# Kernel tuning notes

Measured on AMD Instinct MI355X. Metric: run time of the kernel, lower is better.

The kernel has to match this reference:

```python
import jax, jax.numpy as jnp
import numpy as np

RES = 32  # voxel resolution (init_kwargs)


def setup_inputs() -> dict:
    key = jax.random.key(0)
    k1, k2 = jax.random.split(key)
    B, C, N = 8, 64, 100000
    features = jax.random.normal(k1, (B, C, N), dtype=jnp.float32)
    coords = jax.random.normal(k2, (B, 3, N), dtype=jnp.float32)
    return {"features": features, "coords": coords}


def reference(features, coords):
    # features: [B, C, N], coords: [B, 3, N]
    R = RES
    B, C, N = features.shape
    coords = jax.lax.stop_gradient(coords)  # coords.detach()

    # normalize: center, scale by 2*max point radius, shift to [0,1]
    norm_coords = coords - jnp.mean(coords, axis=2, keepdims=True)
    radius = jnp.linalg.norm(norm_coords, axis=1, keepdims=True)      # [B,1,N]
    scale = jnp.max(radius, axis=2, keepdims=True) * 2.0               # [B,1,1]
    norm_coords = norm_coords / scale + 0.5
    norm_coords = jnp.clip(norm_coords * R, 0, R - 1)                  # [B,3,N]

    vox = jnp.round(norm_coords).astype(jnp.int32)                     # [B,3,N]
    flat = (vox[:, 0] * R + vox[:, 1]) * R + vox[:, 2]                 # [B,N]
    idx = (flat + jnp.arange(B, dtype=jnp.int32)[:, None] * (R * R * R)).reshape(-1)

    feats = features.transpose(0, 2, 1).reshape(B * N, C)              # [B*N, C]
    sums = jax.ops.segment_sum(feats, idx, num_segments=B * R * R * R)
    cnts = jax.ops.segment_sum(jnp.ones((B * N,), features.dtype), idx,
                               num_segments=B * R * R * R)
    avg = sums / jnp.maximum(cnts, 1.0)[:, None]                       # avg voxelize
    grid = avg.reshape(B, R, R, R, C).transpose(0, 4, 1, 2, 3)         # [B,C,R,R,R]
    return grid, norm_coords
```

## Files before the change

kernel.cpp:

```cpp
#include <hip/hip_runtime.h>
#include <hip/hip_bf16.h>

#define RESV 32
#define R3V (RESV * RESV * RESV)
#define R3P1 (R3V + 1)
#define CH 64

__device__ __forceinline__ unsigned short f2bf(float f) {
    __hip_bfloat16 h = __float2bfloat16(f);
    unsigned short u;
    __builtin_memcpy(&u, &h, 2);
    return u;
}
__device__ __forceinline__ unsigned int pkbf(float lo, float hi) {
    return (unsigned int)f2bf(lo) | ((unsigned int)f2bf(hi) << 16);
}
__device__ __forceinline__ float blo(unsigned int u) { return __uint_as_float(u << 16); }
__device__ __forceinline__ float bhi(unsigned int u) { return __uint_as_float(u & 0xffff0000u); }


__global__ void k_sums(const float* __restrict__ coords, float* __restrict__ part,
                       int4* __restrict__ counts4, int N) {
    const int b = blockIdx.y;
    {
        const int g = (blockIdx.y * gridDim.x + blockIdx.x) * blockDim.x + threadIdx.x;
        counts4[g] = make_int4(0, 0, 0, 0);
    }
    const float* cb = coords + (size_t)b * 3 * N;
    float sx = 0.f, sy = 0.f, sz = 0.f;
    for (int n = blockIdx.x * blockDim.x + threadIdx.x; n < N; n += gridDim.x * blockDim.x) {
        sx += cb[n];
        sy += cb[N + n];
        sz += cb[2 * N + n];
    }
    for (int off = 32; off > 0; off >>= 1) {
        sx += __shfl_down(sx, off);
        sy += __shfl_down(sy, off);
        sz += __shfl_down(sz, off);
    }
    __shared__ float red[3][4];
    const int lane = threadIdx.x & 63;
    const int wv   = threadIdx.x >> 6;
    if (lane == 0) { red[0][wv] = sx; red[1][wv] = sy; red[2][wv] = sz; }
    __syncthreads();
    if (threadIdx.x == 0) {
        float tx = 0.f, ty = 0.f, tz = 0.f;
        const int nw = blockDim.x >> 6;
        for (int w = 0; w < nw; ++w) { tx += red[0][w]; ty += red[1][w]; tz += red[2][w]; }
        float* p = part + (b * 32 + blockIdx.x) * 3;
        p[0] = tx; p[1] = ty; p[2] = tz;
    }
}

__global__ void k_maxrad(const float* __restrict__ coords, const float* __restrict__ part,
                         float* __restrict__ maxp, int N) {
    const int b = blockIdx.y;
    __shared__ float sp[96];
    if (threadIdx.x < 96) sp[threadIdx.x] = part[b * 96 + threadIdx.x];
    __syncthreads();
    const float invN = 1.0f / (float)N;
    float mx = 0.f, my = 0.f, mz = 0.f;
    for (int x = 0; x < 32; ++x) { mx += sp[x * 3]; my += sp[x * 3 + 1]; mz += sp[x * 3 + 2]; }
    mx *= invN; my *= invN; mz *= invN;

    const float* cb = coords + (size_t)b * 3 * N;
    float r = 0.f;
    for (int n = blockIdx.x * blockDim.x + threadIdx.x; n < N; n += gridDim.x * blockDim.x) {
        const float dx = cb[n] - mx;
        const float dy = cb[N + n] - my;
        const float dz = cb[2 * N + n] - mz;
        r = fmaxf(r, sqrtf(dx * dx + dy * dy + dz * dz));
    }
    for (int off = 32; off > 0; off >>= 1) r = fmaxf(r, __shfl_down(r, off));
    __shared__ float red[4];
    const int lane = threadIdx.x & 63;
    const int wv   = threadIdx.x >> 6;
    if (lane == 0) red[wv] = r;
    __syncthreads();
    if (threadIdx.x == 0) {
        const int nw = blockDim.x >> 6;
        float t = 0.f;
        for (int w = 0; w < nw; ++w) t = fmaxf(t, red[w]);
        maxp[b * 32 + blockIdx.x] = t;
    }
}

__global__ void k_points(const float* __restrict__ coords, const float* __restrict__ part,
                         const float* __restrict__ maxp,
                         float* __restrict__ norm_out, unsigned int* __restrict__ pk,
                         int* __restrict__ counts, int N) {
    const int b = blockIdx.y;
    __shared__ float sp[96];
    __shared__ float mp[32];
    if (threadIdx.x < 96) sp[threadIdx.x] = part[b * 96 + threadIdx.x];
    if (threadIdx.x < 32) mp[threadIdx.x] = maxp[b * 32 + threadIdx.x];
    __syncthreads();
    const float invN = 1.0f / (float)N;
    float mean[3] = {0.f, 0.f, 0.f};
    float mrad = 0.f;
    for (int x = 0; x < 32; ++x) {
        mean[0] += sp[x * 3]; mean[1] += sp[x * 3 + 1]; mean[2] += sp[x * 3 + 2];
        mrad = fmaxf(mrad, mp[x]);
    }
    const float scale = 2.0f * mrad;

    const int n = blockIdx.x * blockDim.x + threadIdx.x;
    if (n >= N) return;
    const float* cb = coords + (size_t)b * 3 * N;
    float* nb = norm_out + (size_t)b * 3 * N;

    int flat = 0;
#pragma unroll
    for (int d = 0; d < 3; ++d) {
        float nc = (cb[d * N + n] - mean[d] * invN) / scale + 0.5f;
        nc = fminf(fmaxf(nc * (float)RESV, 0.0f), (float)(RESV - 1));
        nb[d * N + n] = nc;
        flat = flat * RESV + (int)rintf(nc);
    }
    const int jl = atomicAdd(&counts[b * R3V + flat], 1);
    pk[(size_t)b * N + n] = ((unsigned int)flat << 17) | (unsigned int)jl;
}

__global__ __launch_bounds__(1024, 1) void k_scan(const int* __restrict__ counts,
                                                  int* __restrict__ start, int N) {
    const int b = blockIdx.x;
    const int t = threadIdx.x;
    const int base  = b * R3V + t * 32;
    const int baseS = b * R3P1 + t * 32;
    int c[32];
    int T = 0;
#pragma unroll
    for (int i = 0; i < 32; ++i) { c[i] = counts[base + i]; T += c[i]; }
    int incl = T;
    const int lane = t & 63;
    for (int off = 1; off < 64; off <<= 1) {
        int y = __shfl_up(incl, off);
        if (lane >= off) incl += y;
    }
    __shared__ int wsum[16];
    __shared__ int wbase[16];
    const int w = t >> 6;
    if (lane == 63) wsum[w] = incl;
    __syncthreads();
    if (t == 0) {
        int run = 0;
        for (int i = 0; i < 16; ++i) { wbase[i] = run; run += wsum[i]; }
    }
    __syncthreads();
    int run = wbase[w] + incl - T;
#pragma unroll
    for (int i = 0; i < 32; ++i) {
        start[baseS + i] = run;
        run += c[i];
    }
    if (t == 1023) start[b * R3P1 + R3V] = run;
}

__global__ __launch_bounds__(1024, 2) void k_transpose_perm(
        const float* __restrict__ feats, const unsigned int* __restrict__ pk,
        const int* __restrict__ startv,
        unsigned int* __restrict__ fTs32, int* __restrict__ voxid, int N) {
    __shared__ unsigned short tile[256][66];
    __shared__ int jrow[256];
    const int b  = blockIdx.y;
    const int n0 = blockIdx.x * 256;
    const int t  = threadIdx.x;
    const float* fb = feats + (size_t)b * 64 * N;

    const int c = t >> 4;
    const int q = t & 15;
    if (n0 + 256 <= N) {
#pragma unroll
        for (int i = 0; i < 4; ++i) {
            const int nn = q * 4 + i * 64;
            const float4 f = *(const float4*)(fb + (size_t)c * N + n0 + nn);
            tile[nn + 0][c] = f2bf(f.x);
            tile[nn + 1][c] = f2bf(f.y);
            tile[nn + 2][c] = f2bf(f.z);
            tile[nn + 3][c] = f2bf(f.w);
        }
    } else {
        for (int i = 0; i < 4; ++i) {
            const int nn = q * 4 + i * 64;
            for (int u = 0; u < 4; ++u) {
                const int n = n0 + nn + u;
                tile[nn + u][c] = f2bf((n < N) ? fb[(size_t)c * N + n] : 0.f);
            }
        }
    }
    if (t < 256) {
        const int n = n0 + t;
        if (n < N) {
            const unsigned int p = pk[(size_t)b * N + n];
            const int v = (int)(p >> 17);
            const int j = startv[(size_t)b * R3P1 + v] + (int)(p & 0x1FFFFu);
            jrow[t] = j;
            voxid[(size_t)b * N + j] = v;
        }
    }
    __syncthreads();

    const int wv   = t >> 6;
    const int lane = t & 63;
    const int lc   = lane & 15;
    const int pr   = lane >> 4;
    uint2* fo2 = (uint2*)fTs32 + (size_t)b * N * 16;
#pragma unroll
    for (int k = 0; k < 4; ++k) {
        const int p = k * 64 + wv * 4 + pr;
        if (n0 + p < N) {
            const uint2 d = *(const uint2*)&tile[p][4 * lc];
            fo2[(size_t)jrow[p] * 16 + lc] = d;
        }
    }
}

__global__ __launch_bounds__(256) void k_gather4(const unsigned int* __restrict__ fTs32,
                                                 const int* __restrict__ voxid,
                                                 const int* __restrict__ startv,
                                                 unsigned int* __restrict__ gridT2,
                                                 int N, int nchunk) {
    const int w     = threadIdx.x >> 6;
    const int lane  = threadIdx.x & 63;
    const int p     = lane >> 4;
    const int lc    = lane & 15;
    const int chunk = blockIdx.x * 4 + w;
    if (chunk >= nchunk) return;
    const int b    = blockIdx.y;
    const int c0   = chunk * CH;
    const int end0 = min(c0 + CH, N);
    const uint2* fb = (const uint2*)(fTs32 + (size_t)b * N * 32);
    const int* vi = voxid  + (size_t)b * N;
    const int* sv = startv + (size_t)b * R3P1;
    uint2* gT = (uint2*)(gridT2) + (size_t)b * R3V * 16;

    int j;
    {
        const int v = vi[c0];
        const int s = sv[v];
        j = (s < c0) ? sv[v + 1] : s;
    }
    while (j < end0) {
        const int v = vi[j];
        const int e = sv[v + 1];
        float a0 = 0.f, a1 = 0.f, a2 = 0.f, a3 = 0.f;
        int r = j + p;
        for (; r + 12 < e; r += 16) {
            const uint2 u0 = fb[(size_t)(r + 0) * 16 + lc];
            const uint2 u1 = fb[(size_t)(r + 4) * 16 + lc];
            const uint2 u2 = fb[(size_t)(r + 8) * 16 + lc];
            const uint2 u3 = fb[(size_t)(r + 12) * 16 + lc];
            a0 += (blo(u0.x) + blo(u1.x)) + (blo(u2.x) + blo(u3.x));
            a1 += (bhi(u0.x) + bhi(u1.x)) + (bhi(u2.x) + bhi(u3.x));
            a2 += (blo(u0.y) + blo(u1.y)) + (blo(u2.y) + blo(u3.y));
            a3 += (bhi(u0.y) + bhi(u1.y)) + (bhi(u2.y) + bhi(u3.y));
        }
        for (; r < e; r += 4) {
            const uint2 u = fb[(size_t)r * 16 + lc];
            a0 += blo(u.x);
            a1 += bhi(u.x);
            a2 += blo(u.y);
            a3 += bhi(u.y);
        }
        a0 += __shfl_xor(a0, 16); a0 += __shfl_xor(a0, 32);
        a1 += __shfl_xor(a1, 16); a1 += __shfl_xor(a1, 32);
        a2 += __shfl_xor(a2, 16); a2 += __shfl_xor(a2, 32);
        a3 += __shfl_xor(a3, 16); a3 += __shfl_xor(a3, 32);
        if (p == 0) {
            gT[(size_t)v * 16 + lc] = make_uint2(pkbf(a0, a1), pkbf(a2, a3));
        }
        j = e;
    }
}

__global__ __launch_bounds__(256) void k_fin(const unsigned int* __restrict__ gridT2,
                                             const int* __restrict__ counts,
                                             float* __restrict__ grid) {
    __shared__ float tile[64][65];
    const int b    = blockIdx.y;
    const int v0   = blockIdx.x * 64;
    const int t    = threadIdx.x;
    const int lane = t & 63;
    const int w    = t >> 6;
    const unsigned int* g = gridT2 + ((size_t)b * R3V + v0) * 32;
#pragma unroll
    for (int k = 0; k < 8; ++k) {
        const int i  = t + k * 256;
        const int v  = i >> 5;
        const int cd = i & 31;
        const unsigned int u = g[i];
        tile[v][2 * cd]     = blo(u);
        tile[v][2 * cd + 1] = bhi(u);
    }
    __syncthreads();
    const int cnt  = counts[(size_t)b * R3V + v0 + lane];
    const float rc = 1.0f / fmaxf((float)cnt, 1.0f);
    const bool occ = cnt > 0;
    float* gb = grid + (size_t)b * 64 * R3V;
#pragma unroll
    for (int k = 0; k < 16; ++k) {
        const int c = w + k * 4;
        gb[(size_t)c * R3V + v0 + lane] = occ ? tile[lane][c] * rc : 0.0f;
    }
}


__device__ __forceinline__ int swz(int v) {
    return v ^ ((v >> 5) & 31) ^ ((v >> 10) & 31);
}

__global__ void k_recip_fb(const int* __restrict__ cnt, float* __restrict__ recip, int total) {
    const int i = blockIdx.x * blockDim.x + threadIdx.x;
    if (i < total) recip[i] = 1.0f / fmaxf((float)cnt[i], 1.0f);
}

__global__ __launch_bounds__(1024, 1) void k_scatter_lds(
        const float* __restrict__ feats, const unsigned int* __restrict__ pk,
        const float* __restrict__ recip, float* __restrict__ grid, int N, int C) {
    extern __shared__ float acc[];
    const int bc  = blockIdx.x;
    const int b   = bc / C;
    const int tid = threadIdx.x;
    for (int i = tid * 4; i < R3V; i += blockDim.x * 4)
        *(float4*)(acc + i) = make_float4(0.f, 0.f, 0.f, 0.f);
    __syncthreads();
    const float* fb = feats + (size_t)bc * N;
    const unsigned int* ib = pk + (size_t)b * N;
    for (int n = tid; n < N; n += blockDim.x) atomicAdd(&acc[swz((int)(ib[n] >> 17))], fb[n]);
    __syncthreads();
    const float* rb = recip + (size_t)b * R3V;
    float*       gb = grid  + (size_t)bc * R3V;
    for (int i = tid; i < R3V; i += blockDim.x)
        gb[i] = acc[swz(i)] * rb[i];
}


extern "C" void kernel_launch(void* const* d_in, const int* in_sizes, int n_in,
                              void* d_out, int out_size, void* d_ws, size_t ws_size,
                              hipStream_t stream) {
    const float* feats  = (const float*)d_in[0];
    const float* coords = (const float*)d_in[1];

    const long long s0 = in_sizes[0], s1 = in_sizes[1];
    const int BC = (int)(((long long)out_size - s1) / R3V);
    const int N  = (int)(s0 / BC);
    const int B  = (int)(s1 / (3LL * N));
    const int C  = BC / B;

    float* out_grid = (float*)d_out;
    float* out_norm = out_grid + (size_t)BC * R3V;

    const size_t BR3 = (size_t)B * R3V;
    const size_t BN  = (size_t)B * N;
    const size_t o_counts = 1024;
    const size_t o_start  = o_counts + BR3;
    const size_t o_recip  = o_start + (size_t)B * R3P1;
    const size_t o_pk     = o_recip + BR3;
    const size_t o_voxid  = o_pk + BN;
    size_t o_gridT = (o_voxid + BN + 63) & ~(size_t)63;
    size_t o_fTs   = (o_gridT + BR3 * 32 + 63) & ~(size_t)63;
    const size_t need = (o_fTs + BN * 32) * sizeof(float);

    float*        ws_part = (float*)d_ws;
    float*        ws_maxp = (float*)d_ws + 768;
    int*          counts  = (int*)d_ws + o_counts;
    int*          startv  = (int*)d_ws + o_start;
    float*        recip   = (float*)d_ws + o_recip;
    unsigned int* pk      = (unsigned int*)d_ws + o_pk;
    int*          voxid   = (int*)d_ws + o_voxid;
    unsigned int* gridT2  = (unsigned int*)((float*)d_ws + o_gridT);
    unsigned int* fTs32   = (unsigned int*)((float*)d_ws + o_fTs);

    const int BLK = 256;
    dim3 gRed(32, B);
    k_sums<<<gRed, BLK, 0, stream>>>(coords, ws_part, (int4*)counts, N);
    k_maxrad<<<gRed, BLK, 0, stream>>>(coords, ws_part, ws_maxp, N);

    dim3 gPts((N + BLK - 1) / BLK, B);
    k_points<<<gPts, BLK, 0, stream>>>(coords, ws_part, ws_maxp, out_norm, pk, counts, N);

    if (ws_size >= need && C == 64) {
        k_scan<<<dim3(B), 1024, 0, stream>>>(counts, startv, N);
        dim3 gT((N + 255) / 256, B);
        k_transpose_perm<<<gT, 1024, 0, stream>>>(feats, pk, startv, fTs32, voxid, N);
        const int nchunk = (N + CH - 1) / CH;
        dim3 gG((nchunk + 3) / 4, B);
        k_gather4<<<gG, 256, 0, stream>>>(fTs32, voxid, startv, gridT2, N, nchunk);
        dim3 gF(R3V / 64, B);
        k_fin<<<gF, 256, 0, stream>>>(gridT2, counts, out_grid);
    } else {
        const int tot = B * R3V;
        k_recip_fb<<<(tot + BLK - 1) / BLK, BLK, 0, stream>>>(counts, recip, tot);
        k_scatter_lds<<<dim3(BC), 1024, R3V * sizeof(float), stream>>>(
            feats, pk, recip, out_grid, N, C);
    }
}
```

Baseline: 224.1 us.

## Vectorize coord reductions and point kernel with float4, widen reduction grid

The reduction kernels (mean sum and max radius) and the per-point normalize/atomic kernel now load coordinates as float4, so each thread handles four points. The max-radius pass compares squared distances and takes one sqrt per block. The partial-reduction grid grows from 32 to 128 blocks per batch for more parallelism, and workspace offsets move to fit the larger partial buffers. Count zeroing is now bounds-checked because the grid no longer matches the count array size. This targets the early small kernels, which are a minor share of total time next to the gather stages.

```diff
diff --git a/kernel.cpp b/kernel.cpp
--- a/kernel.cpp
+++ b/kernel.cpp
@@ -5,6 +5,7 @@
 #define R3V (RESV * RESV * RESV)
 #define R3P1 (R3V + 1)
 #define CH 64
+#define PB 128
 
 __device__ __forceinline__ unsigned short f2bf(float f) {
     __hip_bfloat16 h = __float2bfloat16(f);
@@ -20,15 +21,25 @@
 
 
 __global__ void k_sums(const float* __restrict__ coords, float* __restrict__ part,
-                       int4* __restrict__ counts4, int N) {
+                       int4* __restrict__ counts4, int nInt4, int N) {
     const int b = blockIdx.y;
     {
         const int g = (blockIdx.y * gridDim.x + blockIdx.x) * blockDim.x + threadIdx.x;
-        counts4[g] = make_int4(0, 0, 0, 0);
+        if (g < nInt4) counts4[g] = make_int4(0, 0, 0, 0);
     }
     const float* cb = coords + (size_t)b * 3 * N;
+    const int N4 = N >> 2;
     float sx = 0.f, sy = 0.f, sz = 0.f;
-    for (int n = blockIdx.x * blockDim.x + threadIdx.x; n < N; n += gridDim.x * blockDim.x) {
+    for (int i = blockIdx.x * blockDim.x + threadIdx.x; i < N4; i += gridDim.x * blockDim.x) {
+        const float4 x = ((const float4*)cb)[i];
+        const float4 y = ((const float4*)(cb + N))[i];
+        const float4 z = ((const float4*)(cb + 2 * N))[i];
+        sx += (x.x + x.y) + (x.z + x.w);
+        sy += (y.x + y.y) + (y.z + y.w);
+        sz += (z.x + z.y) + (z.z + z.w);
+    }
+    for (int n = 4 * N4 + blockIdx.x * blockDim.x + threadIdx.x; n < N;
+         n += gridDim.x * blockDim.x) {
         sx += cb[n];
         sy += cb[N + n];
         sz += cb[2 * N + n];
@@ -47,7 +58,7 @@
         float tx = 0.f, ty = 0.f, tz = 0.f;
         const int nw = blockDim.x >> 6;
         for (int w = 0; w < nw; ++w) { tx += red[0][w]; ty += red[1][w]; tz += red[2][w]; }
-        float* p = part + (b * 32 + blockIdx.x) * 3;
+        float* p = part + (b * PB + blockIdx.x) * 3;
         p[0] = tx; p[1] = ty; p[2] = tz;
     }
 }
@@ -55,21 +66,37 @@
 __global__ void k_maxrad(const float* __restrict__ coords, const float* __restrict__ part,
                          float* __restrict__ maxp, int N) {
     const int b = blockIdx.y;
-    __shared__ float sp[96];
-    if (threadIdx.x < 96) sp[threadIdx.x] = part[b * 96 + threadIdx.x];
+    __shared__ float sp[PB * 3];
+    for (int x = threadIdx.x; x < PB * 3; x += blockDim.x) sp[x] = part[b * PB * 3 + x];
     __syncthreads();
     const float invN = 1.0f / (float)N;
     float mx = 0.f, my = 0.f, mz = 0.f;
-    for (int x = 0; x < 32; ++x) { mx += sp[x * 3]; my += sp[x * 3 + 1]; mz += sp[x * 3 + 2]; }
+    for (int x = 0; x < PB; ++x) { mx += sp[x * 3]; my += sp[x * 3 + 1]; mz += sp[x * 3 + 2]; }
     mx *= invN; my *= invN; mz *= invN;
 
     const float* cb = coords + (size_t)b * 3 * N;
+    const int N4 = N >> 2;
     float r = 0.f;
-    for (int n = blockIdx.x * blockDim.x + threadIdx.x; n < N; n += gridDim.x * blockDim.x) {
+    for (int i = blockIdx.x * blockDim.x + threadIdx.x; i < N4; i += gridDim.x * blockDim.x) {
+        const float4 x = ((const float4*)cb)[i];
+        const float4 y = ((const float4*)(cb + N))[i];
+        const float4 z = ((const float4*)(cb + 2 * N))[i];
+        const float dx0 = x.x - mx, dy0 = y.x - my, dz0 = z.x - mz;
+        const float dx1 = x.y - mx, dy1 = y.y - my, dz1 = z.y - mz;
+        const float dx2 = x.z - mx, dy2 = y.z - my, dz2 = z.z - mz;
+        const float dx3 = x.w - mx, dy3 = y.w - my, dz3 = z.w - mz;
+        const float r0 = dx0 * dx0 + dy0 * dy0 + dz0 * dz0;
+        const float r1 = dx1 * dx1 + dy1 * dy1 + dz1 * dz1;
+        const float r2 = dx2 * dx2 + dy2 * dy2 + dz2 * dz2;
+        const float r3 = dx3 * dx3 + dy3 * dy3 + dz3 * dz3;
+        r = fmaxf(r, fmaxf(fmaxf(r0, r1), fmaxf(r2, r3)));
+    }
+    for (int n = 4 * N4 + blockIdx.x * blockDim.x + threadIdx.x; n < N;
+         n += gridDim.x * blockDim.x) {
         const float dx = cb[n] - mx;
         const float dy = cb[N + n] - my;
         const float dz = cb[2 * N + n] - mz;
-        r = fmaxf(r, sqrtf(dx * dx + dy * dy + dz * dz));
+        r = fmaxf(r, dx * dx + dy * dy + dz * dz);
     }
     for (int off = 32; off > 0; off >>= 1) r = fmaxf(r, __shfl_down(r, off));
     __shared__ float red[4];
@@ -81,7 +108,7 @@
         const int nw = blockDim.x >> 6;
         float t = 0.f;
         for (int w = 0; w < nw; ++w) t = fmaxf(t, red[w]);
-        maxp[b * 32 + blockIdx.x] = t;
+        maxp[b * PB + blockIdx.x] = sqrtf(t);
     }
 }
 
@@ -90,35 +117,69 @@
                          float* __restrict__ norm_out, unsigned int* __restrict__ pk,
                          int* __restrict__ counts, int N) {
     const int b = blockIdx.y;
-    __shared__ float sp[96];
-    __shared__ float mp[32];
-    if (threadIdx.x < 96) sp[threadIdx.x] = part[b * 96 + threadIdx.x];
-    if (threadIdx.x < 32) mp[threadIdx.x] = maxp[b * 32 + threadIdx.x];
+    __shared__ float sp[PB * 3];
+    __shared__ float mp[PB];
+    for (int x = threadIdx.x; x < PB * 3; x += blockDim.x) sp[x] = part[b * PB * 3 + x];
+    for (int x = threadIdx.x; x < PB; x += blockDim.x) mp[x] = maxp[b * PB + x];
     __syncthreads();
     const float invN = 1.0f / (float)N;
     float mean[3] = {0.f, 0.f, 0.f};
     float mrad = 0.f;
-    for (int x = 0; x < 32; ++x) {
+    for (int x = 0; x < PB; ++x) {
         mean[0] += sp[x * 3]; mean[1] += sp[x * 3 + 1]; mean[2] += sp[x * 3 + 2];
         mrad = fmaxf(mrad, mp[x]);
     }
     const float scale = 2.0f * mrad;
-
-    const int n = blockIdx.x * blockDim.x + threadIdx.x;
-    if (n >= N) return;
+    const float m0 = mean[0] * invN, m1 = mean[1] * invN, m2 = mean[2] * invN;
+
+    const int i = blockIdx.x * blockDim.x + threadIdx.x;
+    const int n0 = i * 4;
+    if (n0 >= N) return;
     const float* cb = coords + (size_t)b * 3 * N;
     float* nb = norm_out + (size_t)b * 3 * N;
-
-    int flat = 0;
-#pragma unroll
-    for (int d = 0; d < 3; ++d) {
-        float nc = (cb[d * N + n] - mean[d] * invN) / scale + 0.5f;
-        nc = fminf(fmaxf(nc * (float)RESV, 0.0f), (float)(RESV - 1));
-        nb[d * N + n] = nc;
-        flat = flat * RESV + (int)rintf(nc);
-    }
-    const int jl = atomicAdd(&counts[b * R3V + flat], 1);
-    pk[(size_t)b * N + n] = ((unsigned int)flat << 17) | (unsigned int)jl;
+    int* cnts = counts + b * R3V;
+
+    if (n0 + 4 <= N) {
+        float4 cx = ((const float4*)cb)[i];
+        float4 cy = ((const float4*)(cb + N))[i];
+        float4 cz = ((const float4*)(cb + 2 * N))[i];
+        float nx[4] = {cx.x, cx.y, cx.z, cx.w};
+        float ny[4] = {cy.x, cy.y, cy.z, cy.w};
+        float nz[4] = {cz.x, cz.y, cz.z, cz.w};
+        int flat[4];
+#pragma unroll
+        for (int k = 0; k < 4; ++k) {
+            float a = fminf(fmaxf(((nx[k] - m0) / scale + 0.5f) * (float)RESV, 0.0f), (float)(RESV - 1));
+            float bq = fminf(fmaxf(((ny[k] - m1) / scale + 0.5f) * (float)RESV, 0.0f), (float)(RESV - 1));
+            float c = fminf(fmaxf(((nz[k] - m2) / scale + 0.5f) * (float)RESV, 0.0f), (float)(RESV - 1));
+            nx[k] = a; ny[k] = bq; nz[k] = c;
+            flat[k] = ((int)rintf(a) * RESV + (int)rintf(bq)) * RESV + (int)rintf(c);
+        }
+        ((float4*)(nb))[i]         = make_float4(nx[0], nx[1], nx[2], nx[3]);
+        ((float4*)(nb + N))[i]     = make_float4(ny[0], ny[1], ny[2], ny[3]);
+        ((float4*)(nb + 2 * N))[i] = make_float4(nz[0], nz[1], nz[2], nz[3]);
+        uint4 o;
+        o.x = ((unsigned int)flat[0] << 17) | (unsigned int)atomicAdd(&cnts[flat[0]], 1);
+        o.y = ((unsigned int)flat[1] << 17) | (unsigned int)atomicAdd(&cnts[flat[1]], 1);
+        o.z = ((unsigned int)flat[2] << 17) | (unsigned int)atomicAdd(&cnts[flat[2]], 1);
+        o.w = ((unsigned int)flat[3] << 17) | (unsigned int)atomicAdd(&cnts[flat[3]], 1);
+        ((uint4*)(pk + (size_t)b * N))[i] = o;
+    } else {
+        for (int n = n0; n < N; ++n) {
+            int flat = 0;
+            float v[3] = {cb[n], cb[N + n], cb[2 * N + n]};
+            float m[3] = {m0, m1, m2};
+#pragma unroll
+            for (int d = 0; d < 3; ++d) {
+                float nc = fminf(fmaxf(((v[d] - m[d]) / scale + 0.5f) * (float)RESV, 0.0f),
+                                 (float)(RESV - 1));
+                nb[d * N + n] = nc;
+                flat = flat * RESV + (int)rintf(nc);
+            }
+            const int jl = atomicAdd(&cnts[flat], 1);
+            pk[(size_t)b * N + n] = ((unsigned int)flat << 17) | (unsigned int)jl;
+        }
+    }
 }
 
 __global__ __launch_bounds__(1024, 1) void k_scan(const int* __restrict__ counts,
@@ -352,7 +413,7 @@
 
     const size_t BR3 = (size_t)B * R3V;
     const size_t BN  = (size_t)B * N;
-    const size_t o_counts = 1024;
+    const size_t o_counts = 4096;
     const size_t o_start  = o_counts + BR3;
     const size_t o_recip  = o_start + (size_t)B * R3P1;
     const size_t o_pk     = o_recip + BR3;
@@ -362,7 +423,7 @@
     const size_t need = (o_fTs + BN * 32) * sizeof(float);
 
     float*        ws_part = (float*)d_ws;
-    float*        ws_maxp = (float*)d_ws + 768;
+    float*        ws_maxp = (float*)d_ws + 3072;
     int*          counts  = (int*)d_ws + o_counts;
     int*          startv  = (int*)d_ws + o_start;
     float*        recip   = (float*)d_ws + o_recip;
@@ -372,11 +433,13 @@
     unsigned int* fTs32   = (unsigned int*)((float*)d_ws + o_fTs);
 
     const int BLK = 256;
-    dim3 gRed(32, B);
-    k_sums<<<gRed, BLK, 0, stream>>>(coords, ws_part, (int4*)counts, N);
+    const int nInt4 = (int)(BR3 / 4);
+    dim3 gRed(PB, B);
+    k_sums<<<gRed, BLK, 0, stream>>>(coords, ws_part, (int4*)counts, nInt4, N);
     k_maxrad<<<gRed, BLK, 0, stream>>>(coords, ws_part, ws_maxp, N);
 
-    dim3 gPts((N + BLK - 1) / BLK, B);
+    const int nQuads = (N + 3) / 4;
+    dim3 gPts((nQuads + BLK - 1) / BLK, B);
     k_points<<<gPts, BLK, 0, stream>>>(coords, ws_part, ws_maxp, out_norm, pk, counts, N);
 
     if (ws_size >= need && C == 64) {
```

After: 214.0 us. -4.5%, faster.
